# Kernel optimization log

Hardware: AMD Instinct MI355X
Metric: run time of the kernel (lower is better)

Reference implementation:

```python
import jax, jax.numpy as jnp
import numpy as np

N, E, G = 50000, 800000, 500
IN_DIM, EXTRA, HID, HEADS, NCLS = 128, 32, 64, 4, 1
NODE_FEAT2 = HID * HEADS  # 256, input to layer 2
FINAL = NODE_FEAT2 + EXTRA
NODES_PER_GRAPH = N // G  # 100


def gat_layer(h, W, a_l, a_r, b, src, dst, internal_relu):
    # DGL GATConv: fc -> per-head attn logits -> leaky_relu -> edge softmax (over dst) -> weighted sum
    feat = (h @ W).reshape(N, HEADS, HID)            # [N,H,D]
    el = jnp.sum(feat * a_l, axis=-1)                # [N,H]
    er = jnp.sum(feat * a_r, axis=-1)                # [N,H]
    e = jax.nn.leaky_relu(el[src] + er[dst], negative_slope=0.2)  # [E,H]
    m = jax.ops.segment_max(e, dst, num_segments=N)  # [N,H] (stable softmax)
    ex = jnp.exp(e - m[dst])
    denom = jax.ops.segment_sum(ex, dst, num_segments=N)
    alpha = ex / denom[dst]                          # [E,H]
    msg = feat[src] * alpha[:, :, None]              # [E,H,D]
    rst = jax.ops.segment_sum(msg, dst, num_segments=N) + b.reshape(1, HEADS, HID)
    if internal_relu:
        rst = jax.nn.relu(rst)
    return rst


def setup_inputs() -> dict:
    key = jax.random.key(0)
    ks = jax.random.split(key, 20)
    s = 0.05
    inp = {
        "x": jax.random.normal(ks[0], (N, IN_DIM), jnp.float32),
        "desc": jax.random.normal(ks[1], (G, EXTRA), jnp.float32),
        "src": jax.random.randint(ks[2], (E,), 0, N, jnp.int32),
        "dst": jax.random.randint(ks[3], (E,), 0, N, jnp.int32),
        "graph_id": (jnp.arange(N) // NODES_PER_GRAPH).astype(jnp.int32),
        # layer 1 params
        "W1": jax.random.normal(ks[4], (IN_DIM, HEADS * HID), jnp.float32) * s,
        "al1": jax.random.normal(ks[5], (HEADS, HID), jnp.float32) * s,
        "ar1": jax.random.normal(ks[6], (HEADS, HID), jnp.float32) * s,
        "b1": jnp.zeros((HEADS * HID,), jnp.float32),
        # layer 2 params
        "W2": jax.random.normal(ks[7], (NODE_FEAT2, HEADS * HID), jnp.float32) * s,
        "al2": jax.random.normal(ks[8], (HEADS, HID), jnp.float32) * s,
        "ar2": jax.random.normal(ks[9], (HEADS, HID), jnp.float32) * s,
        "b2": jnp.zeros((HEADS * HID,), jnp.float32),
        # MLP head (weights stored [in,out])
        "fc1_w": jax.random.normal(ks[10], (FINAL, HID), jnp.float32) * s,
        "fc1_b": jnp.zeros((HID,), jnp.float32),
        "fc2_w": jax.random.normal(ks[11], (HID, HID // 2), jnp.float32) * s,
        "fc2_b": jnp.zeros((HID // 2,), jnp.float32),
        "out_w": jax.random.normal(ks[12], (HID // 2, NCLS), jnp.float32) * s,
        "out_b": jnp.zeros((NCLS,), jnp.float32),
    }
    return inp


def reference(x, desc, src, dst, graph_id, W1, al1, ar1, b1, W2, al2, ar2, b2,
              fc1_w, fc1_b, fc2_w, fc2_b, out_w, out_b):
    h = gat_layer(x, W1, al1, ar1, b1, src, dst, internal_relu=True)
    h = jax.nn.relu(h.reshape(N, -1))                # flatten heads + outer relu (dropout=0)
    h = gat_layer(h, W2, al2, ar2, b2, src, dst, internal_relu=False)
    h = jax.nn.relu(h.reshape(N, -1))
    # dgl.mean_nodes over batched graph
    hg = jax.ops.segment_sum(h, graph_id, num_segments=G) / float(NODES_PER_GRAPH)  # [G, 256]
    combined = jnp.concatenate([hg, desc], axis=1)   # [G, 288]
    z = jax.nn.relu(combined @ fc1_w + fc1_b)
    z = jax.nn.relu(z @ fc2_w + fc2_b)
    return z @ out_w + out_b                          # [G, 1]
```

## Files before the change

### kernel.cpp

```cpp
#include <hip/hip_runtime.h>
#include <hip/hip_bf16.h>

#define N_NODES 50000
#define N_EDGES 800000
#define N_GRAPHS 500
#define IN_DIM 128
#define EXTRA 32
#define HID 64
#define HEADS 4
#define F2 256
#define NODES_PER_GRAPH 100
#define SCAN_BLOCKS ((N_NODES + 1023) / 1024)
#define GEMM1_BLKS 782
#define SCAT_BLKS 3125

typedef unsigned short u16;
typedef __attribute__((ext_vector_type(8))) short short8;
typedef __attribute__((ext_vector_type(4))) float floatx4;

__device__ __forceinline__ float bf2f(u16 u) {
    union { unsigned int i; float f; } v;
    v.i = ((unsigned int)u) << 16;
    return v.f;
}
__device__ __forceinline__ u16 f2b(float f) {
    __hip_bfloat16 h = __float2bfloat16(f);
    return *reinterpret_cast<u16*>(&h);
}

#define CNT_BLK 3125
#define CVT_BLK 6250
#define RP1_BLK 16
#define RP2_BLK 32
__global__ __launch_bounds__(256) void prep_kernel(const int* __restrict__ dst,
                                                   int* __restrict__ cnt,
                                                   int* __restrict__ rank,
                                                   const float* __restrict__ x,
                                                   u16* __restrict__ xb,
                                                   const float* __restrict__ W1,
                                                   u16* __restrict__ BF1,
                                                   const float* __restrict__ W2,
                                                   u16* __restrict__ BF2) {
    int b = blockIdx.x, t = threadIdx.x;
    if (b < CNT_BLK) {
        int e = b * 256 + t;
        if (e < N_EDGES) rank[e] = atomicAdd(&cnt[dst[e]], 1);
    } else if (b < CNT_BLK + CVT_BLK) {
        int i = (b - CNT_BLK) * 256 + t;
        float4 v = reinterpret_cast<const float4*>(x)[i];
        ushort4 o;
        o.x = f2b(v.x); o.y = f2b(v.y); o.z = f2b(v.z); o.w = f2b(v.w);
        reinterpret_cast<ushort4*>(xb)[i] = o;
    } else {
        const float* W;
        u16* BF;
        int chunk;
        if (b < CNT_BLK + CVT_BLK + RP1_BLK) {
            W = W1; BF = BF1; chunk = (b - CNT_BLK - CVT_BLK) * 4 + (t >> 6);
        } else {
            W = W2; BF = BF2; chunk = (b - CNT_BLK - CVT_BLK - RP1_BLK) * 4 + (t >> 6);
        }
        int l = t & 63;
        int kt = chunk >> 4, ct = chunk & 15;
        int col = ct * 16 + (l & 15);
        int k0 = kt * 32 + 8 * (l >> 4);
        u16* p = BF + (size_t)chunk * 512 + l * 8;
#pragma unroll
        for (int j = 0; j < 8; ++j) p[j] = f2b(W[(size_t)(k0 + j) * 256 + col]);
    }
}

__global__ __launch_bounds__(1024) void scan_block_kernel(const int* __restrict__ cnt,
                                                          int* __restrict__ part,
                                                          int* __restrict__ bsum) {
    __shared__ int buf[1024];
    int b = blockIdx.x, t = threadIdx.x;
    int i = b * 1024 + t;
    buf[t] = (i < N_NODES) ? cnt[i] : 0;
    __syncthreads();
    for (int d = 1; d < 1024; d <<= 1) {
        int add = (t >= d) ? buf[t - d] : 0;
        __syncthreads();
        buf[t] += add;
        __syncthreads();
    }
    if (i < N_NODES) part[i] = buf[t];
    if (t == 1023) bsum[b] = buf[t];
}

__global__ __launch_bounds__(1024) void scan_finalize_kernel(const int* __restrict__ part,
                                                             const int* __restrict__ bsum,
                                                             int* __restrict__ offs,
                                                             int* __restrict__ csr_dst) {
    __shared__ int sb;
    int t = threadIdx.x;
    if (t < 64) {
        int v = (t < blockIdx.x) ? bsum[t] : 0;
#pragma unroll
        for (int d = 32; d > 0; d >>= 1) v += __shfl_xor(v, d);
        if (t == 0) sb = v;
    }
    __syncthreads();
    int sbase = sb;
    int i = blockIdx.x * 1024 + t;
    if (i < N_NODES) {
        int hi = part[i] + sbase;
        offs[i + 1] = hi;
        if (i == 0) offs[0] = 0;
        int lo = (t == 0) ? sbase : part[i - 1] + sbase;
        for (int p = lo; p < hi; ++p) csr_dst[p] = i;
    }
}

template <int K>
__device__ __forceinline__ void gemm_attn_body(int bx, const u16* __restrict__ A,
                                               const u16* __restrict__ BF,
                                               const float* __restrict__ al,
                                               const float* __restrict__ ar,
                                               u16* __restrict__ C,
                                               float* __restrict__ el,
                                               float* __restrict__ er, int M) {
    const int NKT = K / 32;
    __shared__ u16 cxpose[4][16 * 68];
    int t = threadIdx.x;
    int wave = t >> 6, lane = t & 63;
    int l15 = lane & 15, kg = lane >> 4;
    int h = wave;
    int ct0 = h * 4;

    short8 breg[NKT][4];
#pragma unroll
    for (int kt = 0; kt < NKT; ++kt)
#pragma unroll
        for (int c = 0; c < 4; ++c)
            breg[kt][c] = *reinterpret_cast<const short8*>(
                              BF + (size_t)(kt * 16 + ct0 + c) * 512 + lane * 8);

    float alv[4], arv[4];
#pragma unroll
    for (int c = 0; c < 4; ++c) {
        alv[c] = al[(ct0 + c) * 16 + l15];
        arv[c] = ar[(ct0 + c) * 16 + l15];
    }

    u16* cbuf = cxpose[wave];
    for (int rt = 0; rt < 4; ++rt) {
        int row0 = bx * 64 + rt * 16;
        if (row0 >= M) break;
        int arow = row0 + l15; if (arow >= M) arow = M - 1;
        const u16* Ap = A + (size_t)arow * K + kg * 8;

        floatx4 acc[4];
#pragma unroll
        for (int c = 0; c < 4; ++c) acc[c] = (floatx4)0.0f;
#pragma unroll
        for (int kt = 0; kt < NKT; ++kt) {
            short8 a = *reinterpret_cast<const short8*>(Ap + kt * 32);
#pragma unroll
            for (int c = 0; c < 4; ++c)
                acc[c] = __builtin_amdgcn_mfma_f32_16x16x32_bf16(a, breg[kt][c], acc[c], 0, 0, 0);
        }

        floatx4 pl = (floatx4)0.0f, pr = (floatx4)0.0f;
#pragma unroll
        for (int c = 0; c < 4; ++c) {
            pl += acc[c] * alv[c];
            pr += acc[c] * arv[c];
        }
#pragma unroll
        for (int off = 1; off < 16; off <<= 1) {
#pragma unroll
            for (int j = 0; j < 4; ++j) {
                pl[j] += __shfl_xor(pl[j], off);
                pr[j] += __shfl_xor(pr[j], off);
            }
        }
        if (l15 == 0) {
#pragma unroll
            for (int j = 0; j < 4; ++j) {
                int n = row0 + kg * 4 + j;
                if (n < M) { el[n * 4 + h] = pl[j]; er[n * 4 + h] = pr[j]; }
            }
        }

#pragma unroll
        for (int c = 0; c < 4; ++c)
#pragma unroll
            for (int j = 0; j < 4; ++j)
                cbuf[(kg * 4 + j) * 68 + c * 16 + l15] = f2b(acc[c][j]);
#pragma unroll
        for (int it = 0; it < 2; ++it) {
            int r = (lane >> 3) + it * 8;
            int cg = lane & 7;
            int grow = row0 + r;
            if (grow < M) {
                short8 v = *reinterpret_cast<const short8*>(cbuf + r * 68 + cg * 8);
                *reinterpret_cast<short8*>(C + (size_t)grow * 256 + h * 64 + cg * 8) = v;
            }
        }
    }
}

__global__ __launch_bounds__(256) void gemm1_scatter_kernel(const u16* __restrict__ A,
                                                            const u16* __restrict__ BF,
                                                            const float* __restrict__ al,
                                                            const float* __restrict__ ar,
                                                            u16* __restrict__ C,
                                                            float* __restrict__ el,
                                                            float* __restrict__ er,
                                                            const int* __restrict__ src,
                                                            const int* __restrict__ dst,
                                                            const int* __restrict__ offs,
                                                            const int* __restrict__ rank,
                                                            int* __restrict__ csr_src) {
    int b = blockIdx.x;
    int g = b / 5, r = b - g * 5;
    if (r == 0) {
        gemm_attn_body<IN_DIM>(g, A, BF, al, ar, C, el, er, N_NODES);
    } else {
        int e = (b - g - 1) * 256 + threadIdx.x;
        if (e < N_EDGES) {
            int d = dst[e];
            csr_src[offs[d] + rank[e]] = src[e];
        }
    }
}

template <int K>
__global__ __launch_bounds__(256) void gemm_mfma_attn_kernel(const u16* __restrict__ A,
                                                             const u16* __restrict__ BF,
                                                             const float* __restrict__ al,
                                                             const float* __restrict__ ar,
                                                             u16* __restrict__ C,
                                                             float* __restrict__ el,
                                                             float* __restrict__ er, int M) {
    gemm_attn_body<K>(blockIdx.x, A, BF, al, ar, C, el, er, M);
}

__global__ void edge_w_kernel(const int* __restrict__ csr_src, const int* __restrict__ csr_dst,
                              const float* __restrict__ el, const float* __restrict__ er,
                              float* __restrict__ w) {
    int p = blockIdx.x * blockDim.x + threadIdx.x;
    if (p >= N_EDGES) return;
    int s = csr_src[p], d = csr_dst[p];
    float4 l = *reinterpret_cast<const float4*>(&el[s * 4]);
    float4 r = *reinterpret_cast<const float4*>(&er[d * 4]);
    float4 o; float v;
    v = l.x + r.x; v = (v > 0.f) ? v : 0.2f * v; o.x = __expf(v);
    v = l.y + r.y; v = (v > 0.f) ? v : 0.2f * v; o.y = __expf(v);
    v = l.z + r.z; v = (v > 0.f) ? v : 0.2f * v; o.z = __expf(v);
    v = l.w + r.w; v = (v > 0.f) ? v : 0.2f * v; o.w = __expf(v);
    *reinterpret_cast<float4*>(&w[(size_t)p * 4]) = o;
}

__global__ __launch_bounds__(256) void gather_kernel(const u16* __restrict__ feat,
                                                     const float* __restrict__ w,
                                                     const int* __restrict__ offs,
                                                     const int* __restrict__ csr_src,
                                                     const float* __restrict__ bias,
                                                     u16* __restrict__ outb) {
    int n = blockIdx.x * 4 + (threadIdx.x >> 6);
    if (n >= N_NODES) return;
    int lane = threadIdx.x & 63;
    int h = lane >> 4;
    const ushort4* feat4 = reinterpret_cast<const ushort4*>(feat);
    int s0 = offs[n], s1 = offs[n + 1];
    float4 acc = make_float4(0.f, 0.f, 0.f, 0.f);
    float den = 0.f;
    int i = s0;
    for (; i + 4 <= s1; i += 4) {
        int n0 = csr_src[i], n1 = csr_src[i + 1], n2 = csr_src[i + 2], n3 = csr_src[i + 3];
        float x0 = w[(size_t)(i + 0) * 4 + h];
        float x1 = w[(size_t)(i + 1) * 4 + h];
        float x2 = w[(size_t)(i + 2) * 4 + h];
        float x3 = w[(size_t)(i + 3) * 4 + h];
        ushort4 f0 = feat4[(size_t)n0 * 64 + lane];
        ushort4 f1 = feat4[(size_t)n1 * 64 + lane];
        ushort4 f2 = feat4[(size_t)n2 * 64 + lane];
        ushort4 f3 = feat4[(size_t)n3 * 64 + lane];
        acc.x = fmaf(x0, bf2f(f0.x), acc.x); acc.y = fmaf(x0, bf2f(f0.y), acc.y);
        acc.z = fmaf(x0, bf2f(f0.z), acc.z); acc.w = fmaf(x0, bf2f(f0.w), acc.w);
        acc.x = fmaf(x1, bf2f(f1.x), acc.x); acc.y = fmaf(x1, bf2f(f1.y), acc.y);
        acc.z = fmaf(x1, bf2f(f1.z), acc.z); acc.w = fmaf(x1, bf2f(f1.w), acc.w);
        acc.x = fmaf(x2, bf2f(f2.x), acc.x); acc.y = fmaf(x2, bf2f(f2.y), acc.y);
        acc.z = fmaf(x2, bf2f(f2.z), acc.z); acc.w = fmaf(x2, bf2f(f2.w), acc.w);
        acc.x = fmaf(x3, bf2f(f3.x), acc.x); acc.y = fmaf(x3, bf2f(f3.y), acc.y);
        acc.z = fmaf(x3, bf2f(f3.z), acc.z); acc.w = fmaf(x3, bf2f(f3.w), acc.w);
        den += (x0 + x1) + (x2 + x3);
    }
    for (; i < s1; ++i) {
        int s = csr_src[i];
        float x = w[(size_t)i * 4 + h];
        ushort4 f = feat4[(size_t)s * 64 + lane];
        acc.x = fmaf(x, bf2f(f.x), acc.x); acc.y = fmaf(x, bf2f(f.y), acc.y);
        acc.z = fmaf(x, bf2f(f.z), acc.z); acc.w = fmaf(x, bf2f(f.w), acc.w);
        den += x;
    }
    float inv = (s1 > s0) ? 1.f / den : 0.f;
    float4 bv = reinterpret_cast<const float4*>(bias)[lane];
    ushort4 o;
    o.x = f2b(fmaxf(fmaf(acc.x, inv, bv.x), 0.f));
    o.y = f2b(fmaxf(fmaf(acc.y, inv, bv.y), 0.f));
    o.z = f2b(fmaxf(fmaf(acc.z, inv, bv.z), 0.f));
    o.w = f2b(fmaxf(fmaf(acc.w, inv, bv.w), 0.f));
    reinterpret_cast<ushort4*>(outb)[(size_t)n * 64 + lane] = o;
}

__global__ __launch_bounds__(256) void head_kernel(const u16* __restrict__ h2,
                                                   const float* __restrict__ desc,
                                                   const float* __restrict__ fc1_w,
                                                   const float* __restrict__ fc1_b,
                                                   const float* __restrict__ fc2_w,
                                                   const float* __restrict__ fc2_b,
                                                   const float* __restrict__ out_w,
                                                   const float* __restrict__ out_b,
                                                   float* __restrict__ out) {
    __shared__ float comb[288];
    __shared__ float z1[64];
    __shared__ float z2[32];
    int g = blockIdx.x, t = threadIdx.x;
    const u16* base = h2 + (size_t)g * NODES_PER_GRAPH * 256;
    float s0 = 0.f, s1 = 0.f, s2 = 0.f, s3 = 0.f;
    for (int i = 0; i < NODES_PER_GRAPH; i += 4) {
        s0 += bf2f(base[(size_t)(i + 0) * 256 + t]);
        s1 += bf2f(base[(size_t)(i + 1) * 256 + t]);
        s2 += bf2f(base[(size_t)(i + 2) * 256 + t]);
        s3 += bf2f(base[(size_t)(i + 3) * 256 + t]);
    }
    comb[t] = ((s0 + s1) + (s2 + s3)) * (1.f / NODES_PER_GRAPH);
    if (t < EXTRA) comb[256 + t] = desc[g * EXTRA + t];
    __syncthreads();
    if (t < 64) {
        float a = fc1_b[t];
        for (int i = 0; i < 288; ++i) a += comb[i] * fc1_w[i * 64 + t];
        z1[t] = fmaxf(a, 0.f);
    }
    __syncthreads();
    if (t < 32) {
        float a = fc2_b[t];
        for (int i = 0; i < 64; ++i) a += z1[i] * fc2_w[i * 32 + t];
        z2[t] = fmaxf(a, 0.f);
    }
    __syncthreads();
    if (t == 0) {
        float a = out_b[0];
        for (int i = 0; i < 32; ++i) a += z2[i] * out_w[i];
        out[g] = a;
    }
}

extern "C" void kernel_launch(void* const* d_in, const int* in_sizes, int n_in,
                              void* d_out, int out_size, void* d_ws, size_t ws_size,
                              hipStream_t stream) {
    const float* x     = (const float*)d_in[0];
    const float* desc  = (const float*)d_in[1];
    const int*   src   = (const int*)d_in[2];
    const int*   dst   = (const int*)d_in[3];
    const float* W1    = (const float*)d_in[5];
    const float* al1   = (const float*)d_in[6];
    const float* ar1   = (const float*)d_in[7];
    const float* b1    = (const float*)d_in[8];
    const float* W2    = (const float*)d_in[9];
    const float* al2   = (const float*)d_in[10];
    const float* ar2   = (const float*)d_in[11];
    const float* b2    = (const float*)d_in[12];
    const float* fc1_w = (const float*)d_in[13];
    const float* fc1_b = (const float*)d_in[14];
    const float* fc2_w = (const float*)d_in[15];
    const float* fc2_b = (const float*)d_in[16];
    const float* out_w = (const float*)d_in[17];
    const float* out_b = (const float*)d_in[18];
    float* out = (float*)d_out;

    char* ws = (char*)d_ws;
    size_t off = 0;
    auto alloc = [&](size_t bytes) -> void* {
        void* p = ws + off;
        off = (off + bytes + 255) & ~(size_t)255;
        return p;
    };
    u16*   xb      = (u16*)alloc((size_t)N_NODES * IN_DIM * 2);
    u16*   featb   = (u16*)alloc((size_t)N_NODES * 256 * 2);
    u16*   h1b     = (u16*)alloc((size_t)N_NODES * 256 * 2);
    u16*   h2b     = (u16*)alloc((size_t)N_NODES * 256 * 2);
    u16*   BF1     = (u16*)alloc((size_t)IN_DIM * 256 * 2);
    u16*   BF2     = (u16*)alloc((size_t)F2 * 256 * 2);
    float* el      = (float*)alloc((size_t)N_NODES * 4 * 4);
    float* er      = (float*)alloc((size_t)N_NODES * 4 * 4);
    int*   offs    = (int*)alloc((size_t)(N_NODES + 1) * 4);
    int*   cnt     = (int*)alloc((size_t)N_NODES * 4);
    int*   part    = (int*)alloc((size_t)N_NODES * 4);
    int*   bsum    = (int*)alloc(64 * 4);
    int*   csr_src = (int*)alloc((size_t)N_EDGES * 4);
    int*   csr_dst = (int*)alloc((size_t)N_EDGES * 4);
    int*   rankb   = (int*)alloc((size_t)N_EDGES * 4);
    float* wbuf    = (float*)alloc((size_t)N_EDGES * 4 * 4);

    hipMemsetAsync(cnt, 0, (size_t)N_NODES * 4, stream);
    prep_kernel<<<CNT_BLK + CVT_BLK + RP1_BLK + RP2_BLK, 256, 0, stream>>>(
        dst, cnt, rankb, x, xb, W1, BF1, W2, BF2);
    scan_block_kernel<<<SCAN_BLOCKS, 1024, 0, stream>>>(cnt, part, bsum);
    scan_finalize_kernel<<<SCAN_BLOCKS, 1024, 0, stream>>>(part, bsum, offs, csr_dst);

    int eb = (N_EDGES + 255) / 256;
    int ngb = (N_NODES + 3) / 4;
    gemm1_scatter_kernel<<<GEMM1_BLKS + SCAT_BLKS, 256, 0, stream>>>(
        xb, BF1, al1, ar1, featb, el, er, src, dst, offs, rankb, csr_src);
    edge_w_kernel<<<eb, 256, 0, stream>>>(csr_src, csr_dst, el, er, wbuf);
    gather_kernel<<<ngb, 256, 0, stream>>>(featb, wbuf, offs, csr_src, b1, h1b);
    gemm_mfma_attn_kernel<F2><<<(N_NODES + 63) / 64, 256, 0, stream>>>(
        h1b, BF2, al2, ar2, featb, el, er, N_NODES);
    edge_w_kernel<<<eb, 256, 0, stream>>>(csr_src, csr_dst, el, er, wbuf);
    gather_kernel<<<ngb, 256, 0, stream>>>(featb, wbuf, offs, csr_src, b2, h2b);
    head_kernel<<<N_GRAPHS, 256, 0, stream>>>(h2b, desc, fc1_w, fc1_b, fc2_w, fc2_b,
                                              out_w, out_b, out);
}
```

Measured before the change: 257.4 us.

## Compute layer-2 attention logits in gather1 and overlap GEMM2 with edge weights

Precomputes W2·al2 and W2·ar2 in a tiny prep kernel, then has the layer-1 gather kernel compute layer-2 el/er directly from the fp32 post-ReLU features with a wavefront reduction. Because the logits no longer depend on GEMM2, the second GEMM and the layer-2 edge-weight computation run as interleaved blocks of one launch, removing a serialization point and a launch. The cost is extra shared memory and shuffle work in the gather. The logits now come from fp32 features rather than bf16 GEMM output, so they differ slightly numerically.

```diff
diff --git a/kernel.cpp b/kernel.cpp
--- a/kernel.cpp
+++ b/kernel.cpp
@@ -11,7 +11,7 @@
 #define F2 256
 #define NODES_PER_GRAPH 100
 #define SCAN_BLOCKS ((N_NODES + 1023) / 1024)
-#define GEMM1_BLKS 782
+#define GEMM_BLKS 782
 #define SCAT_BLKS 3125
 
 typedef unsigned short u16;
@@ -26,6 +26,24 @@
 __device__ __forceinline__ u16 f2b(float f) {
     __hip_bfloat16 h = __float2bfloat16(f);
     return *reinterpret_cast<u16*>(&h);
+}
+
+__global__ __launch_bounds__(256) void prep0_kernel(const float* __restrict__ W2,
+                                                    const float* __restrict__ al2,
+                                                    const float* __restrict__ ar2,
+                                                    float* __restrict__ Wal2) {
+    int c = threadIdx.x;
+    const float* wr = W2 + (size_t)c * 256;
+    float acc[8] = {0.f};
+#pragma unroll
+    for (int h = 0; h < 4; ++h)
+        for (int j = 0; j < 64; ++j) {
+            float wv = wr[h * 64 + j];
+            acc[h * 2 + 0] = fmaf(wv, al2[h * 64 + j], acc[h * 2 + 0]);
+            acc[h * 2 + 1] = fmaf(wv, ar2[h * 64 + j], acc[h * 2 + 1]);
+        }
+#pragma unroll
+    for (int q = 0; q < 8; ++q) Wal2[c * 8 + q] = acc[q];
 }
 
 #define CNT_BLK 3125
@@ -201,6 +219,23 @@
     }
 }
 
+__device__ __forceinline__ void edge_w_body(int e, const int* __restrict__ csr_src,
+                                            const int* __restrict__ csr_dst,
+                                            const float* __restrict__ el,
+                                            const float* __restrict__ er,
+                                            float* __restrict__ w) {
+    if (e >= N_EDGES) return;
+    int s = csr_src[e], d = csr_dst[e];
+    float4 l = *reinterpret_cast<const float4*>(&el[s * 4]);
+    float4 r = *reinterpret_cast<const float4*>(&er[d * 4]);
+    float4 o; float v;
+    v = l.x + r.x; v = (v > 0.f) ? v : 0.2f * v; o.x = __expf(v);
+    v = l.y + r.y; v = (v > 0.f) ? v : 0.2f * v; o.y = __expf(v);
+    v = l.z + r.z; v = (v > 0.f) ? v : 0.2f * v; o.z = __expf(v);
+    v = l.w + r.w; v = (v > 0.f) ? v : 0.2f * v; o.w = __expf(v);
+    *reinterpret_cast<float4*>(&w[(size_t)e * 4]) = o;
+}
+
 __global__ __launch_bounds__(256) void gemm1_scatter_kernel(const u16* __restrict__ A,
                                                             const u16* __restrict__ BF,
                                                             const float* __restrict__ al,
@@ -226,31 +261,114 @@
     }
 }
 
-template <int K>
-__global__ __launch_bounds__(256) void gemm_mfma_attn_kernel(const u16* __restrict__ A,
-                                                             const u16* __restrict__ BF,
-                                                             const float* __restrict__ al,
-                                                             const float* __restrict__ ar,
-                                                             u16* __restrict__ C,
-                                                             float* __restrict__ el,
-                                                             float* __restrict__ er, int M) {
-    gemm_attn_body<K>(blockIdx.x, A, BF, al, ar, C, el, er, M);
+__global__ __launch_bounds__(256) void gemm2_edgew_kernel(const u16* __restrict__ A,
+                                                          const u16* __restrict__ BF,
+                                                          const float* __restrict__ al,
+                                                          const float* __restrict__ ar,
+                                                          u16* __restrict__ C,
+                                                          float* __restrict__ el_dummy,
+                                                          float* __restrict__ er_dummy,
+                                                          const int* __restrict__ csr_src,
+                                                          const int* __restrict__ csr_dst,
+                                                          const float* __restrict__ el2,
+                                                          const float* __restrict__ er2,
+                                                          float* __restrict__ w) {
+    int b = blockIdx.x;
+    int g = b / 5, r = b - g * 5;
+    if (r == 0) {
+        gemm_attn_body<F2>(g, A, BF, al, ar, C, el_dummy, er_dummy, N_NODES);
+    } else {
+        int e = (b - g - 1) * 256 + threadIdx.x;
+        edge_w_body(e, csr_src, csr_dst, el2, er2, w);
+    }
 }
 
 __global__ void edge_w_kernel(const int* __restrict__ csr_src, const int* __restrict__ csr_dst,
                               const float* __restrict__ el, const float* __restrict__ er,
                               float* __restrict__ w) {
-    int p = blockIdx.x * blockDim.x + threadIdx.x;
-    if (p >= N_EDGES) return;
-    int s = csr_src[p], d = csr_dst[p];
-    float4 l = *reinterpret_cast<const float4*>(&el[s * 4]);
-    float4 r = *reinterpret_cast<const float4*>(&er[d * 4]);
-    float4 o; float v;
-    v = l.x + r.x; v = (v > 0.f) ? v : 0.2f * v; o.x = __expf(v);
-    v = l.y + r.y; v = (v > 0.f) ? v : 0.2f * v; o.y = __expf(v);
-    v = l.z + r.z; v = (v > 0.f) ? v : 0.2f * v; o.z = __expf(v);
-    v = l.w + r.w; v = (v > 0.f) ? v : 0.2f * v; o.w = __expf(v);
-    *reinterpret_cast<float4*>(&w[(size_t)p * 4]) = o;
+    edge_w_body(blockIdx.x * blockDim.x + threadIdx.x, csr_src, csr_dst, el, er, w);
+}
+
+__global__ __launch_bounds__(256) void gather1_kernel(const u16* __restrict__ feat,
+                                                      const float* __restrict__ w,
+                                                      const int* __restrict__ offs,
+                                                      const int* __restrict__ csr_src,
+                                                      const float* __restrict__ bias,
+                                                      const float* __restrict__ Wal2,
+                                                      u16* __restrict__ outb,
+                                                      float* __restrict__ el2,
+                                                      float* __restrict__ er2) {
+    __shared__ float wal[256][8];
+    {
+        const float4* src4 = reinterpret_cast<const float4*>(Wal2 + threadIdx.x * 8);
+        *reinterpret_cast<float4*>(&wal[threadIdx.x][0]) = src4[0];
+        *reinterpret_cast<float4*>(&wal[threadIdx.x][4]) = src4[1];
+    }
+    __syncthreads();
+    int n = blockIdx.x * 4 + (threadIdx.x >> 6);
+    if (n >= N_NODES) return;
+    int lane = threadIdx.x & 63;
+    int h = lane >> 4;
+    const ushort4* feat4 = reinterpret_cast<const ushort4*>(feat);
+    int s0 = offs[n], s1 = offs[n + 1];
+    float4 acc = make_float4(0.f, 0.f, 0.f, 0.f);
+    float den = 0.f;
+    int i = s0;
+    for (; i + 4 <= s1; i += 4) {
+        int n0 = csr_src[i], n1 = csr_src[i + 1], n2 = csr_src[i + 2], n3 = csr_src[i + 3];
+        float x0 = w[(size_t)(i + 0) * 4 + h];
+        float x1 = w[(size_t)(i + 1) * 4 + h];
+        float x2 = w[(size_t)(i + 2) * 4 + h];
+        float x3 = w[(size_t)(i + 3) * 4 + h];
+        ushort4 f0 = feat4[(size_t)n0 * 64 + lane];
+        ushort4 f1 = feat4[(size_t)n1 * 64 + lane];
+        ushort4 f2 = feat4[(size_t)n2 * 64 + lane];
+        ushort4 f3 = feat4[(size_t)n3 * 64 + lane];
+        acc.x = fmaf(x0, bf2f(f0.x), acc.x); acc.y = fmaf(x0, bf2f(f0.y), acc.y);
+        acc.z = fmaf(x0, bf2f(f0.z), acc.z); acc.w = fmaf(x0, bf2f(f0.w), acc.w);
+        acc.x = fmaf(x1, bf2f(f1.x), acc.x); acc.y = fmaf(x1, bf2f(f1.y), acc.y);
+        acc.z = fmaf(x1, bf2f(f1.z), acc.z); acc.w = fmaf(x1, bf2f(f1.w), acc.w);
+        acc.x = fmaf(x2, bf2f(f2.x), acc.x); acc.y = fmaf(x2, bf2f(f2.y), acc.y);
+        acc.z = fmaf(x2, bf2f(f2.z), acc.z); acc.w = fmaf(x2, bf2f(f2.w), acc.w);
+        acc.x = fmaf(x3, bf2f(f3.x), acc.x); acc.y = fmaf(x3, bf2f(f3.y), acc.y);
+        acc.z = fmaf(x3, bf2f(f3.z), acc.z); acc.w = fmaf(x3, bf2f(f3.w), acc.w);
+        den += (x0 + x1) + (x2 + x3);
+    }
+    for (; i < s1; ++i) {
+        int s = csr_src[i];
+        float x = w[(size_t)i * 4 + h];
+        ushort4 f = feat4[(size_t)s * 64 + lane];
+        acc.x = fmaf(x, bf2f(f.x), acc.x); acc.y = fmaf(x, bf2f(f.y), acc.y);
+        acc.z = fmaf(x, bf2f(f.z), acc.z); acc.w = fmaf(x, bf2f(f.w), acc.w);
+        den += x;
+    }
+    float inv = (s1 > s0) ? 1.f / den : 0.f;
+    float4 bv = reinterpret_cast<const float4*>(bias)[lane];
+    float4 rr;
+    rr.x = fmaxf(fmaf(acc.x, inv, bv.x), 0.f);
+    rr.y = fmaxf(fmaf(acc.y, inv, bv.y), 0.f);
+    rr.z = fmaxf(fmaf(acc.z, inv, bv.z), 0.f);
+    rr.w = fmaxf(fmaf(acc.w, inv, bv.w), 0.f);
+    ushort4 o;
+    o.x = f2b(rr.x); o.y = f2b(rr.y); o.z = f2b(rr.z); o.w = f2b(rr.w);
+    reinterpret_cast<ushort4*>(outb)[(size_t)n * 64 + lane] = o;
+
+    int c0 = lane * 4;
+    float p[8];
+#pragma unroll
+    for (int q = 0; q < 8; ++q)
+        p[q] = rr.x * wal[c0][q] + rr.y * wal[c0 + 1][q] +
+               rr.z * wal[c0 + 2][q] + rr.w * wal[c0 + 3][q];
+#pragma unroll
+    for (int off = 1; off < 64; off <<= 1)
+#pragma unroll
+        for (int q = 0; q < 8; ++q) p[q] += __shfl_xor(p[q], off);
+    if (lane == 0) {
+        float4 evl = make_float4(p[0], p[2], p[4], p[6]);
+        float4 evr = make_float4(p[1], p[3], p[5], p[7]);
+        *reinterpret_cast<float4*>(&el2[n * 4]) = evl;
+        *reinterpret_cast<float4*>(&er2[n * 4]) = evr;
+    }
 }
 
 __global__ __launch_bounds__(256) void gather_kernel(const u16* __restrict__ feat,
@@ -387,6 +505,9 @@
     u16*   BF2     = (u16*)alloc((size_t)F2 * 256 * 2);
     float* el      = (float*)alloc((size_t)N_NODES * 4 * 4);
     float* er      = (float*)alloc((size_t)N_NODES * 4 * 4);
+    float* el2     = (float*)alloc((size_t)N_NODES * 4 * 4);
+    float* er2     = (float*)alloc((size_t)N_NODES * 4 * 4);
+    float* Wal2    = (float*)alloc((size_t)256 * 8 * 4);
     int*   offs    = (int*)alloc((size_t)(N_NODES + 1) * 4);
     int*   cnt     = (int*)alloc((size_t)N_NODES * 4);
     int*   part    = (int*)alloc((size_t)N_NODES * 4);
@@ -397,6 +518,7 @@
     float* wbuf    = (float*)alloc((size_t)N_EDGES * 4 * 4);
 
     hipMemsetAsync(cnt, 0, (size_t)N_NODES * 4, stream);
+    prep0_kernel<<<1, 256, 0, stream>>>(W2, al2, ar2, Wal2);
     prep_kernel<<<CNT_BLK + CVT_BLK + RP1_BLK + RP2_BLK, 256, 0, stream>>>(
         dst, cnt, rankb, x, xb, W1, BF1, W2, BF2);
     scan_block_kernel<<<SCAN_BLOCKS, 1024, 0, stream>>>(cnt, part, bsum);
@@ -404,13 +526,13 @@
 
     int eb = (N_EDGES + 255) / 256;
     int ngb = (N_NODES + 3) / 4;
-    gemm1_scatter_kernel<<<GEMM1_BLKS + SCAT_BLKS, 256, 0, stream>>>(
+    gemm1_scatter_kernel<<<GEMM_BLKS + SCAT_BLKS, 256, 0, stream>>>(
         xb, BF1, al1, ar1, featb, el, er, src, dst, offs, rankb, csr_src);
     edge_w_kernel<<<eb, 256, 0, stream>>>(csr_src, csr_dst, el, er, wbuf);
-    gather_kernel<<<ngb, 256, 0, stream>>>(featb, wbuf, offs, csr_src, b1, h1b);
-    gemm_mfma_attn_kernel<F2><<<(N_NODES + 63) / 64, 256, 0, stream>>>(
-        h1b, BF2, al2, ar2, featb, el, er, N_NODES);
-    edge_w_kernel<<<eb, 256, 0, stream>>>(csr_src, csr_dst, el, er, wbuf);
+    gather1_kernel<<<ngb, 256, 0, stream>>>(featb, wbuf, offs, csr_src, b1, Wal2,
+                                            h1b, el2, er2);
+    gemm2_edgew_kernel<<<GEMM_BLKS + SCAT_BLKS, 256, 0, stream>>>(
+        h1b, BF2, al2, ar2, featb, el, er, csr_src, csr_dst, el2, er2, wbuf);
     gather_kernel<<<ngb, 256, 0, stream>>>(featb, wbuf, offs, csr_src, b2, h2b);
     head_kernel<<<N_GRAPHS, 256, 0, stream>>>(h2b, desc, fc1_w, fc1_b, fc2_w, fc2_b,
                                               out_w, out_b, out);
```

Result: slower. 294.4 us (+14.4%).
